# Kernel optimization log

Measured on AMD Instinct MI355X. Metric: run time of the kernel, lower is better.

## Reference

```python
import jax, jax.numpy as jnp
import numpy as np

THRESHOLD = 0.35      # overlap_thresh
NEGPOS_RATIO = 7
VAR0, VAR1 = 0.1, 0.2  # self.variance


def make_priors():
    # Standard RetinaFace 640x640 anchor grid -> 16800 priors (cx, cy, w, h)
    img = 640
    steps = [8, 16, 32]
    min_sizes = [[16, 32], [64, 128], [256, 512]]
    out = []
    for step, ms in zip(steps, min_sizes):
        f = img // step
        ii, jj = np.meshgrid(np.arange(f), np.arange(f), indexing="ij")
        cx = ((jj + 0.5) * step / img).ravel().astype(np.float32)
        cy = ((ii + 0.5) * step / img).ravel().astype(np.float32)
        for m in ms:
            s = np.full_like(cx, m / img)
            out.append(np.stack([cx, cy, s, s], axis=-1))
    return jnp.asarray(np.concatenate(out, axis=0), dtype=jnp.float32)


def jaccard(a, b):
    # a: [O,4] point-form gt boxes, b: [P,4] point-form priors -> IoU [O,P]
    lt = jnp.maximum(a[:, None, :2], b[None, :, :2])
    rb = jnp.minimum(a[:, None, 2:], b[None, :, 2:])
    wh = jnp.clip(rb - lt, 0.0)
    inter = wh[..., 0] * wh[..., 1]
    area_a = ((a[:, 2] - a[:, 0]) * (a[:, 3] - a[:, 1]))[:, None]
    area_b = ((b[:, 2] - b[:, 0]) * (b[:, 3] - b[:, 1]))[None, :]
    return inter / (area_a + area_b - inter)


def setup_inputs() -> dict:
    key = jax.random.key(0)
    ks = jax.random.split(key, 7)
    B, P, O = 64, 16800, 64
    loc_data = jax.random.normal(ks[0], (B, P, 4), jnp.float32)
    conf_data = jax.random.normal(ks[1], (B, P, 2), jnp.float32)
    landm_data = jax.random.normal(ks[2], (B, P, 10), jnp.float32)
    priors = make_priors()
    # targets: [B, O, 15] = [xmin ymin xmax ymax | 10 landmark coords | label]
    c = jax.random.uniform(ks[3], (B, O, 2), minval=0.15, maxval=0.85)
    wh = jax.random.uniform(ks[4], (B, O, 2), minval=0.05, maxval=0.3)
    boxes = jnp.concatenate([jnp.clip(c - wh / 2, 1e-3, 0.999),
                             jnp.clip(c + wh / 2, 1e-3, 0.999)], axis=-1)
    landms = jax.random.uniform(ks[5], (B, O, 10))
    lab = jnp.where(jax.random.uniform(ks[6], (B, O, 1)) < 0.8, 1.0, -1.0)
    targets = jnp.concatenate([boxes, landms, lab], axis=-1).astype(jnp.float32)
    return {"loc_data": loc_data, "conf_data": conf_data,
            "landm_data": landm_data, "priors": priors, "targets": targets}


def _smooth_l1(x):
    ax = jnp.abs(x)
    return jnp.where(ax < 1.0, 0.5 * ax * ax, ax - 0.5)


def reference(loc_data, conf_data, landm_data, priors, targets):
    B, P, C = conf_data.shape
    O = targets.shape[1]
    priors_pf = jnp.concatenate([priors[:, :2] - priors[:, 2:] * 0.5,
                                 priors[:, :2] + priors[:, 2:] * 0.5], axis=1)

    def match_one(t):
        truths = t[:, :4]
        landms = t[:, 4:14]
        labels = t[:, 14].astype(jnp.int32)
        ov = jaccard(truths, priors_pf)               # [O,P]
        bp_ov = ov.max(axis=1)                         # best prior per truth
        bp_idx = jnp.argmax(ov, axis=1)
        valid = bp_ov >= 0.2                           # RetinaFace gt filter
        bt_ov = ov.max(axis=0)                         # best truth per prior
        bt_idx = jnp.argmax(ov, axis=0)
        # index_fill_(best_prior_idx, 2) for valid gts, ensure best prior kept
        bt_ov = bt_ov.at[bp_idx].set(jnp.where(valid, 2.0, bt_ov[bp_idx]))
        bt_idx = bt_idx.at[bp_idx].set(jnp.arange(O))
        matched = truths[bt_idx]                       # [P,4] point form
        conf = labels[bt_idx]
        conf = jnp.where(bt_ov < THRESHOLD, 0, conf)
        # encode loc target
        g_cxcy = ((matched[:, :2] + matched[:, 2:]) * 0.5 - priors[:, :2]) / (VAR0 * priors[:, 2:])
        g_wh = jnp.log((matched[:, 2:] - matched[:, :2]) / priors[:, 2:]) / VAR1
        loc = jnp.concatenate([g_cxcy, g_wh], axis=1)
        # encode landmark target (5 points)
        ml = landms[bt_idx].reshape(P, 5, 2)
        lm = ((ml - priors[:, None, :2]) / (VAR0 * priors[:, None, 2:])).reshape(P, 10)
        any_valid = jnp.any(valid)                     # early-return branch of match()
        return (jnp.where(any_valid, loc, 0.0),
                jnp.where(any_valid, conf, 0),
                jnp.where(any_valid, lm, 0.0))

    loc_t, conf_t, landm_t = jax.vmap(match_one)(targets)
    loc_t = jax.lax.stop_gradient(loc_t)       # targets built from .data in torch
    landm_t = jax.lax.stop_gradient(landm_t)

    # landmark loss over conf_t > 0
    pos1 = conf_t > 0
    N1 = jnp.maximum(pos1.sum().astype(jnp.float32), 1.0)
    loss_landm = jnp.sum(jnp.where(pos1[..., None], _smooth_l1(landm_data - landm_t), 0.0))

    # localization loss over conf_t != 0 (labels -1 and 1 both positive)
    pos = conf_t != 0
    conf_t1 = jnp.where(pos, 1, conf_t)        # conf_t[pos] = 1 -> values in {0,1}
    loss_l = jnp.sum(jnp.where(pos[..., None], _smooth_l1(loc_data - loc_t), 0.0))

    # hard negative mining
    lse = jax.nn.logsumexp(conf_data, axis=2)                       # [B,P]
    picked = jnp.take_along_axis(conf_data, conf_t1[..., None], axis=2)[..., 0]
    ce_all = lse - picked                                            # per-anchor CE
    rank_score = jnp.where(pos, 0.0, ce_all)
    loss_idx = jnp.argsort(-rank_score, axis=1)
    idx_rank = jnp.argsort(loss_idx, axis=1)
    num_pos = pos.sum(axis=1, keepdims=True)
    num_neg = jnp.minimum(NEGPOS_RATIO * num_pos, P - 1)
    neg = idx_rank < num_neg
    union = pos | neg
    loss_c = jnp.sum(jnp.where(union, ce_all, 0.0))

    N = jnp.maximum(num_pos.sum().astype(jnp.float32), 1.0)
    return loss_l / N, loss_c / N, loss_landm / N1
```

## Files before the change

### kernel.cpp

```cpp
#include <hip/hip_runtime.h>
#include <math.h>

#define B 64
#define P 16800
#define O 64
#define THRESH 0.35f
#define VALID_T 0.2f
#define HB 2048
#define HSHIFT 21
#define AREA_M 0.34f
#define CCAP 4096
#define MULT 2
#define CHB (MULT * 256)
#define NB2 ((P + CHB - 1) / CHB)
#define KD1B (B * NB2)
#define KB2B (B * O / 4)

__device__ __forceinline__ float smooth_l1(float x) {
    float ax = fabsf(x);
    return ax < 1.f ? 0.5f * ax * ax : ax - 0.5f;
}
__device__ __forceinline__ float lse2(float c0, float c1) {
    float m = fmaxf(c0, c1);
    return m + __logf(__expf(c0 - m) + __expf(c1 - m));
}
__device__ __forceinline__ void iou_upd(float4 t, float area_a,
                                        float px1, float py1, float px2, float py2,
                                        float area_b,
                                        float& bnum, float& bden, int& bio, int o) {
    float w = fmaxf(fminf(t.z, px2) - fmaxf(t.x, px1), 0.f);
    float h = fmaxf(fminf(t.w, py2) - fmaxf(t.y, py1), 0.f);
    float inter = w * h;
    float den = area_a + area_b - inter;
    if (inter * bden > bnum * den) { bnum = inter; bden = den; bio = o; }
}
__device__ __forceinline__ float wave_sum(float v) {
#pragma unroll
    for (int s = 32; s > 0; s >>= 1) v += __shfl_down(v, s, 64);
    return v;
}
__device__ __forceinline__ int wave_sum_i(int v) {
#pragma unroll
    for (int s = 32; s > 0; s >>= 1) v += __shfl_down(v, s, 64);
    return v;
}
__device__ __forceinline__ float wave_min(float v) {
#pragma unroll
    for (int s = 32; s > 0; s >>= 1) v = fminf(v, __shfl_xor(v, s, 64));
    return v;
}
__device__ __forceinline__ float wave_max(float v) {
#pragma unroll
    for (int s = 32; s > 0; s >>= 1) v = fmaxf(v, __shfl_xor(v, s, 64));
    return v;
}
__device__ __forceinline__ int wave_sufscan(int v, int lane) {
#pragma unroll
    for (int s = 1; s < 64; s <<= 1) {
        int o = __shfl_down(v, s, 64);
        if (lane + s < 64) v += o;
    }
    return v;
}

__global__ void __launch_bounds__(256) kMain(
        const float* __restrict__ loc_data,
        const float* __restrict__ landm_data, const float* __restrict__ priors,
        const float* __restrict__ targets,
        unsigned char* __restrict__ pflag,
        int* __restrict__ num_pos,
        float* __restrict__ gsum, int* __restrict__ np1_tot,
        unsigned long long* __restrict__ bp_final) {
    if (blockIdx.x >= KD1B) {
        int pair = (blockIdx.x - KD1B) * 4 + (threadIdx.x >> 6);
        int lane = threadIdx.x & 63;
        int o = pair & (O - 1);
        int b = pair >> 6;
        const float* tt = &targets[(b * O + o) * 15];
        float tx1 = tt[0], ty1 = tt[1], tx2 = tt[2], ty2 = tt[3];
        float area_a = (tx2 - tx1) * (ty2 - ty1);
        float4 tb = make_float4(tx1, ty1, tx2, ty2);
        float bn = 0.f, bd = 1.f;
        unsigned bp = 0u;
        const int fs[6]   = {80, 80, 40, 40, 20, 20};
        const int ms[6]   = {16, 32, 64, 128, 256, 512};
        const int base[6] = {0, 6400, 12800, 14400, 16000, 16400};
#pragma unroll
        for (int c = 0; c < 6; ++c) {
            int f = fs[c];
            float inv = (float)f;
            float h = (float)ms[c] * (0.5f / 640.f);
            int j0 = (int)floorf((tx1 - h) * inv - 0.5f) - 1; if (j0 < 0) j0 = 0;
            int j1 = (int)ceilf((tx2 + h) * inv - 0.5f) + 1;  if (j1 > f - 1) j1 = f - 1;
            int i0 = (int)floorf((ty1 - h) * inv - 0.5f) - 1; if (i0 < 0) i0 = 0;
            int i1 = (int)ceilf((ty2 + h) * inv - 0.5f) + 1;  if (i1 > f - 1) i1 = f - 1;
            if (j1 < j0 || i1 < i0) continue;
            int nj = j1 - j0 + 1;
            int n = (i1 - i0 + 1) * nj;
            float rcp_nj = 1.0f / (float)nj;
            for (int idx = lane; idx < n; idx += 64) {
                int ii = (int)((float)idx * rcp_nj);
                int jj = idx - ii * nj;
                if (jj < 0) { ii--; jj += nj; } else if (jj >= nj) { ii++; jj -= nj; }
                int p = base[c] + (i0 + ii) * f + (j0 + jj);
                float4 q = ((const float4*)priors)[p];
                float px1 = q.x - q.z * 0.5f, py1 = q.y - q.w * 0.5f;
                float px2 = q.x + q.z * 0.5f, py2 = q.y + q.w * 0.5f;
                float areab = (px2 - px1) * (py2 - py1);
                float w = fmaxf(fminf(tb.z, px2) - fmaxf(tb.x, px1), 0.f);
                float hh = fmaxf(fminf(tb.w, py2) - fmaxf(tb.y, py1), 0.f);
                float inter = w * hh;
                float den = area_a + areab - inter;
                float l = bn * den, r = inter * bd;
                if (r > l) { bn = inter; bd = den; bp = (unsigned)p; }
            }
        }
#pragma unroll
        for (int s = 32; s > 0; s >>= 1) {
            float no = __shfl_xor(bn, s, 64), dd = __shfl_xor(bd, s, 64);
            unsigned po = __shfl_xor(bp, s, 64);
            float l = bn * dd, r = no * bd;
            bool take = (r > l) || (r == l && po < bp);
            if (take) { bn = no; bd = dd; bp = po; }
        }
        if (lane == 0) {
            float iou = bn / bd;
            bp_final[b * O + o] = ((unsigned long long)__float_as_uint(iou) << 32)
                                | (unsigned)(0xFFFFFFFFu - bp);
        }
        return;
    }
    int blk = blockIdx.x % NB2;
    int b = blockIdx.x / NB2;
    int p0 = blk * CHB;
    __shared__ float traw[O * 15];
    __shared__ float4 t4[O];
    __shared__ float ta[O], lab[O];
    __shared__ float4 wbb[4];
    __shared__ float2 wab[4];
    __shared__ int alist[O];
    __shared__ int s_cnt;
    __shared__ float wredf[2][4];
    __shared__ int wredi[2][4];
    int tid = threadIdx.x;
    if (tid < O * 15 / 4)
        ((float4*)traw)[tid] = ((const float4*)(targets + (size_t)b * O * 15))[tid];
    float px1[MULT], py1[MULT], px2[MULT], py2[MULT], areab[MULT];
    float4 pr4[MULT];
    float bnum[MULT], bden[MULT]; int bi[MULT]; bool act[MULT];
    float bx1 = 1e30f, by1 = 1e30f, bx2 = -1e30f, by2 = -1e30f;
    float amn = 1e30f, amx = -1e30f;
#pragma unroll
    for (int mi = 0; mi < MULT; ++mi) {
        int p = p0 + mi * 256 + tid;
        act[mi] = (p < P);
        int pc = act[mi] ? p : (P - 1);
        float4 q = ((const float4*)priors)[pc];
        pr4[mi] = q;
        px1[mi] = q.x - q.z * 0.5f; py1[mi] = q.y - q.w * 0.5f;
        px2[mi] = q.x + q.z * 0.5f; py2[mi] = q.y + q.w * 0.5f;
        areab[mi] = (px2[mi] - px1[mi]) * (py2[mi] - py1[mi]);
        bx1 = fminf(bx1, px1[mi]); by1 = fminf(by1, py1[mi]);
        bx2 = fmaxf(bx2, px2[mi]); by2 = fmaxf(by2, py2[mi]);
        amn = fminf(amn, areab[mi]); amx = fmaxf(amx, areab[mi]);
        bnum[mi] = 0.f; bden[mi] = 1.f; bi[mi] = 0;
    }
    bx1 = wave_min(bx1); by1 = wave_min(by1);
    bx2 = wave_max(bx2); by2 = wave_max(by2);
    amn = wave_min(amn); amx = wave_max(amx);
    int wid = tid >> 6, lid = tid & 63;
    if (lid == 0) { wbb[wid] = make_float4(bx1, by1, bx2, by2); wab[wid] = make_float2(amn, amx); }
    __syncthreads();
    if (tid < 64) {
        const float* tr = &traw[tid * 15];
        float a0 = tr[0], a1 = tr[1], a2 = tr[2], a3 = tr[3];
        float4 t = make_float4(a0, a1, a2, a3);
        t4[tid] = t;
        float Aa = (a2 - a0) * (a3 - a1);
        ta[tid] = Aa;
        lab[tid] = tr[14];
        float ux1 = fminf(fminf(wbb[0].x, wbb[1].x), fminf(wbb[2].x, wbb[3].x));
        float uy1 = fminf(fminf(wbb[0].y, wbb[1].y), fminf(wbb[2].y, wbb[3].y));
        float ux2 = fmaxf(fmaxf(wbb[0].z, wbb[1].z), fmaxf(wbb[2].z, wbb[3].z));
        float uy2 = fmaxf(fmaxf(wbb[0].w, wbb[1].w), fmaxf(wbb[2].w, wbb[3].w));
        float bmn = fminf(fminf(wab[0].x, wab[1].x), fminf(wab[2].x, wab[3].x));
        float bmx = fmaxf(fmaxf(wab[0].y, wab[1].y), fmaxf(wab[2].y, wab[3].y));
        bool pass = (fminf(t.z, ux2) - fmaxf(t.x, ux1) > 0.f) &&
                    (fminf(t.w, uy2) - fmaxf(t.y, uy1) > 0.f) &&
                    (Aa >= AREA_M * bmn) && (bmx >= AREA_M * Aa);
        unsigned long long mask = __ballot(pass);
        if (tid == 0) s_cnt = __popcll(mask);
        if (pass) {
            int pos = __popcll(mask & ((1ull << tid) - 1ull));
            alist[pos] = tid;
        }
    }
    __syncthreads();
    int cnt = s_cnt;
    for (int li = 0; li < cnt; ++li) {
        int o = alist[li];
        float4 t = t4[o];
        float w0 = fminf(t.z, bx2) - fmaxf(t.x, bx1);
        float h0 = fminf(t.w, by2) - fmaxf(t.y, by1);
        if (w0 <= 0.f || h0 <= 0.f) continue;
        float Aa = ta[o];
#pragma unroll
        for (int mi = 0; mi < MULT; ++mi) {
            float Ap = areab[mi];
            if (Aa >= AREA_M * Ap && Ap >= AREA_M * Aa)
                iou_upd(t, Aa, px1[mi], py1[mi], px2[mi], py2[mi], Ap,
                        bnum[mi], bden[mi], bi[mi], o);
        }
    }
    float ll = 0.f, llm = 0.f;
    int cp = 0, cp1 = 0;
#pragma unroll
    for (int mi = 0; mi < MULT; ++mi) {
        if (!act[mi]) continue;
        int p = p0 + mi * 256 + tid;
        float best = bnum[mi] / bden[mi];
        int conf = (best >= THRESH) ? (int)lab[bi[mi]] : 0;
        bool pos = conf != 0;
        pflag[(size_t)b * P + p] = pos ? 1 : 0;
        if (pos) {
            cp++;
            int ti = bi[mi];
            float cx = pr4[mi].x, cy = pr4[mi].y, sw = pr4[mi].z, sh = pr4[mi].w;
            float4 t = t4[ti];
            float gx = ((t.x + t.z) * 0.5f - cx) / (0.1f * sw);
            float gy = ((t.y + t.w) * 0.5f - cy) / (0.1f * sh);
            float gw = logf((t.z - t.x) / sw) / 0.2f;
            float gh = logf((t.w - t.y) / sh) / 0.2f;
            const float* ld = &loc_data[(size_t)(b * P + p) * 4];
            ll += smooth_l1(ld[0] - gx) + smooth_l1(ld[1] - gy) +
                  smooth_l1(ld[2] - gw) + smooth_l1(ld[3] - gh);
            if (conf > 0) {
                cp1++;
                const float* lmd = &landm_data[(size_t)(b * P + p) * 10];
                const float* lmt = &traw[ti * 15 + 4];
                for (int k5 = 0; k5 < 5; ++k5) {
                    float lx = (lmt[k5 * 2 + 0] - cx) / (0.1f * sw);
                    float ly = (lmt[k5 * 2 + 1] - cy) / (0.1f * sh);
                    llm += smooth_l1(lmd[k5 * 2 + 0] - lx) + smooth_l1(lmd[k5 * 2 + 1] - ly);
                }
            }
        }
    }
    float s_ll = wave_sum(ll), s_llm = wave_sum(llm);
    int s_cp = wave_sum_i(cp), s_cp1 = wave_sum_i(cp1);
    if (lid == 0) {
        wredf[0][wid] = s_ll; wredf[1][wid] = s_llm;
        wredi[0][wid] = s_cp; wredi[1][wid] = s_cp1;
    }
    __syncthreads();
    if (tid == 0) {
        float ll_t = wredf[0][0] + wredf[0][1] + wredf[0][2] + wredf[0][3];
        float llm_t = wredf[1][0] + wredf[1][1] + wredf[1][2] + wredf[1][3];
        int cp_t = wredi[0][0] + wredi[0][1] + wredi[0][2] + wredi[0][3];
        int cp1_t = wredi[1][0] + wredi[1][1] + wredi[1][2] + wredi[1][3];
        if (ll_t != 0.f)  atomicAdd(&gsum[0], ll_t);
        if (llm_t != 0.f) atomicAdd(&gsum[1], llm_t);
        if (cp_t)  atomicAdd(&num_pos[b], cp_t);
        if (cp1_t) atomicAdd(np1_tot, cp1_t);
    }
}

__global__ void __launch_bounds__(1024) kTail(
        const float* __restrict__ priors, const float* __restrict__ targets,
        const float* __restrict__ loc_data, const float* __restrict__ conf_data,
        const float* __restrict__ landm_data,
        const unsigned long long* __restrict__ bp_final,
        const unsigned char* __restrict__ pflag,
        const int* __restrict__ num_pos,
        float* __restrict__ gsum, int* __restrict__ np1_tot, int* __restrict__ np_tot,
        float* __restrict__ lossc_tot, int* __restrict__ done,
        float* __restrict__ out) {
    __shared__ __align__(16) unsigned lrow[P];
    __shared__ float4 t4[O];
    __shared__ float ta[O], lab[O];
    __shared__ int sp[O];
    __shared__ int lh[HB];
    __shared__ int chunkSum[256];
    __shared__ int suf[257];
    __shared__ int waveTot[4];
    __shared__ int hist2[256];
    __shared__ unsigned lcand[CCAP];
    __shared__ int s_np, s_bin0, s_kk0, s_bin, s_kk, s_cnt;
    __shared__ float wredf[16];
    __shared__ int wredi[16];
    __shared__ float s_cepw[16];
    __shared__ float s_sumgt;

    int b = blockIdx.x;
    int tid = threadIdx.x;
    for (int i = tid; i < HB; i += 1024) lh[i] = 0;
    if (tid == 0) s_cnt = 0;
    int p = 0, v = 0;
    if (tid < O) {
        const float* tt = &targets[(b * O + tid) * 15];
        float4 tj = make_float4(tt[0], tt[1], tt[2], tt[3]);
        t4[tid] = tj;
        ta[tid] = (tj.z - tj.x) * (tj.w - tj.y);
        lab[tid] = tt[14];
        unsigned long long kpk = bp_final[b * O + tid];
        p = (int)(0xFFFFFFFFu - (unsigned)(kpk & 0xFFFFFFFFu));
        float iou = __uint_as_float((unsigned)(kpk >> 32));
        v = (iou >= VALID_T) ? 1 : 0;
        sp[tid] = p;
    }
    __syncthreads();
    const float4* c4 = (const float4*)(conf_data + (size_t)b * P * 2);
    const uchar4* f4v = (const uchar4*)(pflag + (size_t)b * P);
    float cep = 0.f;
    for (int i = tid; i < P / 4; i += 1024) {
        float4 a = c4[2 * i];
        float4 c = c4[2 * i + 1];
        uchar4 fl = f4v[i];
        float l0 = lse2(a.x, a.y), l1 = lse2(a.z, a.w);
        float l2 = lse2(c.x, c.y), l3 = lse2(c.z, c.w);
        bool q0 = fl.x != 0, q1 = fl.y != 0, q2 = fl.z != 0, q3 = fl.w != 0;
        float ce0 = l0 - (q0 ? a.y : a.x);
        float ce1 = l1 - (q1 ? a.w : a.z);
        float ce2 = l2 - (q2 ? c.y : c.x);
        float ce3 = l3 - (q3 ? c.w : c.z);
        if (q0) cep += ce0;
        if (q1) cep += ce1;
        if (q2) cep += ce2;
        if (q3) cep += ce3;
        unsigned u0 = __float_as_uint(q0 ? 0.f : ce0);
        unsigned u1 = __float_as_uint(q1 ? 0.f : ce1);
        unsigned u2 = __float_as_uint(q2 ? 0.f : ce2);
        unsigned u3 = __float_as_uint(q3 ? 0.f : ce3);
        ((uint4*)lrow)[i] = make_uint4(u0, u1, u2, u3);
        atomicAdd(&lh[u0 >> HSHIFT], 1);
        atomicAdd(&lh[u1 >> HSHIFT], 1);
        atomicAdd(&lh[u2 >> HSHIFT], 1);
        atomicAdd(&lh[u3 >> HSHIFT], 1);
    }
    {
        float sc = wave_sum(cep);
        if ((tid & 63) == 0) s_cepw[tid >> 6] = sc;
    }
    __syncthreads();
    int dnp = 0, dn1 = 0;
    float dll = 0.f, dllm = 0.f, dce = 0.f;
    if (tid < O) {
        int j = tid;
        bool winner = true;
        for (int jj = j + 1; jj < O; ++jj)
            if (sp[jj] == p) { winner = false; break; }
        if (winner) {
            float4 q = ((const float4*)priors)[p];
            float px1 = q.x - q.z * 0.5f, py1 = q.y - q.w * 0.5f;
            float px2 = q.x + q.z * 0.5f, py2 = q.y + q.w * 0.5f;
            float areab = (px2 - px1) * (py2 - py1);
            float bnum = 0.f, bden = 1.f; int bi = 0;
            for (int o = 0; o < O; ++o) {
                float Aa = ta[o];
                if (Aa >= AREA_M * areab && areab >= AREA_M * Aa)
                    iou_upd(t4[o], Aa, px1, py1, px2, py2, areab, bnum, bden, bi, o);
            }
            float best = bnum / bden;
            float ov_new = v ? 2.0f : best;
            int conf_old = (best >= THRESH) ? (int)lab[bi] : 0;
            int conf_new = (ov_new >= THRESH) ? (int)lab[j] : 0;
            float2 c01 = ((const float2*)conf_data)[b * P + p];
            float c0 = c01.x, c1 = c01.y;
            float lse = lse2(c0, c1);
            bool po = conf_old != 0, pn = conf_new != 0;
            float ceo = lse - (po ? c1 : c0), cen = lse - (pn ? c1 : c0);
            float rvo = po ? 0.f : ceo, rvn = pn ? 0.f : cen;
            if (__float_as_uint(rvo) != __float_as_uint(rvn)) {
                lrow[p] = __float_as_uint(rvn);
                int bo = __float_as_uint(rvo) >> HSHIFT, bn = __float_as_uint(rvn) >> HSHIFT;
                if (bo != bn) { atomicAdd(&lh[bn], 1); atomicAdd(&lh[bo], -1); }
            }
            const float* ld = &loc_data[(size_t)(b * P + p) * 4];
            auto enc_ll = [&](int ti) -> float {
                float4 t = t4[ti];
                float gx = ((t.x + t.z) * 0.5f - q.x) / (0.1f * q.z);
                float gy = ((t.y + t.w) * 0.5f - q.y) / (0.1f * q.w);
                float gw = logf((t.z - t.x) / q.z) / 0.2f;
                float gh = logf((t.w - t.y) / q.w) / 0.2f;
                return smooth_l1(ld[0] - gx) + smooth_l1(ld[1] - gy) +
                       smooth_l1(ld[2] - gw) + smooth_l1(ld[3] - gh);
            };
            if (po) dll -= enc_ll(bi);
            if (pn) dll += enc_ll(j);
            dce = (pn ? cen : 0.f) - (po ? ceo : 0.f);
            dnp = (int)pn - (int)po;
            const float* lmd = &landm_data[(size_t)(b * P + p) * 10];
            auto enc_lm = [&](int ti) -> float {
                const float* lmt = &targets[(b * O + ti) * 15 + 4];
                float sum = 0.f;
                for (int k5 = 0; k5 < 5; ++k5) {
                    float lx = (lmt[k5 * 2 + 0] - q.x) / (0.1f * q.z);
                    float ly = (lmt[k5 * 2 + 1] - q.y) / (0.1f * q.w);
                    sum += smooth_l1(lmd[k5 * 2 + 0] - lx) + smooth_l1(lmd[k5 * 2 + 1] - ly);
                }
                return sum;
            };
            if (conf_old > 0) dllm -= enc_lm(bi);
            if (conf_new > 0) dllm += enc_lm(j);
            dn1 = (int)(conf_new > 0) - (int)(conf_old > 0);
        }
    }
    float pce_reg = 0.f;
    if (tid < 64) {
        float r_ll = wave_sum(dll), r_lm = wave_sum(dllm), r_ce = wave_sum(dce);
        int r_np = wave_sum_i(dnp), r_n1 = wave_sum_i(dn1);
        if (tid == 0) {
            if (r_ll != 0.f) atomicAdd(&gsum[0], r_ll);
            if (r_lm != 0.f) atomicAdd(&gsum[1], r_lm);
            float cep_tot = 0.f;
            for (int i = 0; i < 16; ++i) cep_tot += s_cepw[i];
            pce_reg = cep_tot + r_ce;
            int np = num_pos[b] + r_np;
            s_np = np;
            atomicAdd(np_tot, np);
            if (r_n1) atomicAdd(np1_tot, r_n1);
        }
    }
    __syncthreads();
    int k = s_np * 7;
    if (k > P - 1) k = P - 1;
    if (tid < 256) {
        int cs = 0;
#pragma unroll
        for (int i = 0; i < HB / 256; ++i) cs += lh[tid * (HB / 256) + i];
        chunkSum[tid] = cs;
    }
    if (tid == 0) { s_bin0 = (k <= 0) ? -1 : 0; s_kk0 = (k <= 0) ? 0 : k; }
    __syncthreads();
    {
        int lane = tid & 63;
        int vv = (tid < 256) ? chunkSum[tid] : 0;
        vv = wave_sufscan(vv, lane);
        if (tid < 256 && lane == 0) waveTot[tid >> 6] = vv;
        __syncthreads();
        if (tid < 256) {
            int after = 0;
            for (int g = (tid >> 6) + 1; g < 4; ++g) after += waveTot[g];
            suf[tid] = vv + after;
            if (tid == 0) suf[256] = 0;
        }
        __syncthreads();
        if (k > 0 && tid < 256) {
            if (suf[tid] >= k && suf[tid + 1] < k) {
                int cum = suf[tid + 1];
                for (int i = HB / 256 - 1; i >= 0; --i) {
                    int hv = lh[tid * (HB / 256) + i];
                    if (cum + hv >= k) { s_bin0 = tid * (HB / 256) + i; s_kk0 = k - cum; break; }
                    cum += hv;
                }
            }
        }
    }
    __syncthreads();
    int bin = s_bin0;
    int kk0 = s_kk0;
    float topk_b = 0.f;
    if (bin >= 0) {
        if (tid < 256) hist2[tid] = 0;
        __syncthreads();
        unsigned lo_bound = ((unsigned)(bin + 1)) << HSHIFT;
        float sumgt = 0.f;
        for (int i = tid; i < P / 4; i += 1024) {
            uint4 u4 = ((const uint4*)lrow)[i];
#define TAIL_H(u) { if ((u) >= lo_bound) sumgt += __uint_as_float(u); \
                    else if (((u) >> HSHIFT) == (unsigned)bin) { \
                        int idx = atomicAdd(&s_cnt, 1); \
                        if (idx < CCAP) lcand[idx] = (u); \
                        atomicAdd(&hist2[((u) >> 13) & 255], 1); } }
            TAIL_H(u4.x) TAIL_H(u4.y) TAIL_H(u4.z) TAIL_H(u4.w)
#undef TAIL_H
        }
        float sg = wave_sum(sumgt);
        if ((tid & 63) == 0) wredf[tid >> 6] = sg;
        __syncthreads();
        if (tid == 0) {
            float t = 0.f;
            for (int i = 0; i < 16; ++i) t += wredf[i];
            s_sumgt = t;
        }
        {
            int lane = tid & 63, nb = 256;
            int vv = (tid < nb) ? hist2[tid] : 0;
            vv = wave_sufscan(vv, lane);
            if (tid < nb && lane == 0) waveTot[tid >> 6] = vv;
            __syncthreads();
            if (tid < nb) {
                int after = 0;
                for (int g = (tid >> 6) + 1; g < 4; ++g) after += waveTot[g];
                suf[tid] = vv + after;
                if (tid == 0) suf[nb] = 0;
            }
            __syncthreads();
            if (tid < nb) {
                if (suf[tid] >= kk0 && suf[tid + 1] < kk0) { s_bin = tid; s_kk = kk0 - suf[tid + 1]; }
            }
            __syncthreads();
        }
        unsigned pref = (((unsigned)bin) << HSHIFT) | (((unsigned)s_bin) << 13);
        unsigned resolved = (0xFFFFFFFFu << HSHIFT) | (255u << 13);
        int kk = s_kk;
        int m = s_cnt;
        bool useG = (m > CCAP);
        for (int pass = 0; pass < 2; ++pass) {
            int sh = pass == 0 ? 5 : 0;
            int nb = pass == 0 ? 256 : 32;
            if (tid < nb) hist2[tid] = 0;
            __syncthreads();
            if (!useG) {
                for (int i = tid; i < m; i += 1024) {
                    unsigned u = lcand[i];
                    if ((u & resolved) == pref) atomicAdd(&hist2[(u >> sh) & (nb - 1)], 1);
                }
            } else {
                for (int pp = tid; pp < P; pp += 1024) {
                    unsigned u = lrow[pp];
                    if ((u & resolved) == pref) atomicAdd(&hist2[(u >> sh) & (nb - 1)], 1);
                }
            }
            __syncthreads();
            {
                int lane = tid & 63;
                int vv = (tid < nb) ? hist2[tid] : 0;
                vv = wave_sufscan(vv, lane);
                if (tid < nb && lane == 0) waveTot[tid >> 6] = vv;
                __syncthreads();
                int ng = (nb + 63) >> 6;
                if (tid < nb) {
                    int after = 0;
                    for (int g = (tid >> 6) + 1; g < ng; ++g) after += waveTot[g];
                    suf[tid] = vv + after;
                    if (tid == 0) suf[nb] = 0;
                }
                __syncthreads();
                if (tid < nb) {
                    if (suf[tid] >= kk && suf[tid + 1] < kk) { s_bin = tid; s_kk = kk - suf[tid + 1]; }
                }
                __syncthreads();
            }
            pref |= ((unsigned)s_bin) << sh;
            resolved |= (unsigned)(nb - 1) << sh;
            kk = s_kk;
            __syncthreads();
        }
        float tv = __uint_as_float(pref);
        float sumS = 0.f; int cntS = 0;
        for (int pp = tid; pp < P; pp += 1024) {
            unsigned u = lrow[pp];
            if ((u >> HSHIFT) == (unsigned)bin) {
                float val = __uint_as_float(u);
                if (val > tv) { sumS += val; cntS++; }
            }
        }
        float s2 = wave_sum(sumS); int c2 = wave_sum_i(cntS);
        if ((tid & 63) == 0) { wredf[tid >> 6] = s2; wredi[tid >> 6] = c2; }
        __syncthreads();
        if (tid == 0) {
            float st = 0.f; int ct = 0;
            for (int i = 0; i < 16; ++i) { st += wredf[i]; ct += wredi[i]; }
            topk_b = s_sumgt + st + (float)(kk0 - ct) * tv;
        }
    }
    if (tid == 0) {
        atomicAdd(lossc_tot, pce_reg + topk_b);
        __threadfence();
        int old = atomicAdd(done, 1);
        if (old == B - 1) {
            float g0 = atomicAdd(&gsum[0], 0.f);
            float g1 = atomicAdd(&gsum[1], 0.f);
            float lc = atomicAdd(lossc_tot, 0.f);
            int np = atomicAdd(np_tot, 0);
            int n1 = atomicAdd(np1_tot, 0);
            float N = fmaxf((float)np, 1.f);
            float N1 = fmaxf((float)n1, 1.f);
            out[0] = g0 / N;
            out[1] = lc / N;
            out[2] = g1 / N1;
        }
    }
}

extern "C" void kernel_launch(void* const* d_in, const int* in_sizes, int n_in,
                              void* d_out, int out_size, void* d_ws, size_t ws_size,
                              hipStream_t stream) {
    const float* loc_data   = (const float*)d_in[0];
    const float* conf_data  = (const float*)d_in[1];
    const float* landm_data = (const float*)d_in[2];
    const float* priors     = (const float*)d_in[3];
    const float* targets    = (const float*)d_in[4];
    float* out = (float*)d_out;

    char* ws = (char*)d_ws;
    size_t off = 0;
    auto alloc = [&](size_t bytes) -> void* {
        void* pp = ws + off;
        off += (bytes + 255) & ~(size_t)255;
        return pp;
    };
    unsigned char* pflag = (unsigned char*)alloc((size_t)B * P);
    unsigned long long* bp_final = (unsigned long long*)alloc((size_t)B * O * 8);
    size_t acc_bytes = (size_t)(B * 4 + 64);
    char* acc = (char*)alloc(acc_bytes);
    int*   num_pos      = (int*)acc;
    float* gsum         = (float*)(acc + B * 4);
    int*   np1_tot      = (int*)(acc + B * 4 + 8);
    int*   np_tot       = (int*)(acc + B * 4 + 12);
    float* lossc_tot    = (float*)(acc + B * 4 + 16);
    int*   done         = (int*)(acc + B * 4 + 20);

    hipMemsetAsync(acc, 0, acc_bytes, stream);
    kMain<<<dim3(KD1B + KB2B), dim3(256), 0, stream>>>(loc_data, landm_data,
                                                       priors, targets, pflag,
                                                       num_pos, gsum, np1_tot,
                                                       bp_final);
    kTail<<<dim3(B), dim3(1024), 0, stream>>>(priors, targets, loc_data, conf_data,
                                              landm_data, bp_final, pflag,
                                              num_pos, gsum, np1_tot, np_tot,
                                              lossc_tot, done, out);
}
```

Before: 165.4 us.

## Process two images per block, per-wave ballot culling, privatized histograms, single-wave select

The matching kernel now handles two batch rows per block and reuses the prior geometry and its per-wave bounding boxes across both rows. Candidate GT culling moves from a block-level shared list to a per-wave ballot mask over each MULT slice, which drops several barriers. The top-k kernel splits its histogram into four copies to cut atomic contention, then merges them. It also replaces the multi-barrier suffix-scan bin selection with a single-wavefront routine. Trade-offs are half as many matching blocks, so less parallelism, plus extra shared memory for the histogram copies.

```diff
diff --git a/kernel.cpp b/kernel.cpp
--- a/kernel.cpp
+++ b/kernel.cpp
@@ -11,9 +11,10 @@
 #define AREA_M 0.34f
 #define CCAP 4096
 #define MULT 2
+#define RPB 2
 #define CHB (MULT * 256)
 #define NB2 ((P + CHB - 1) / CHB)
-#define KD1B (B * NB2)
+#define KD1B ((B / RPB) * NB2)
 #define KB2B (B * O / 4)
 
 __device__ __forceinline__ float smooth_l1(float x) {
@@ -61,6 +62,27 @@
         if (lane + s < 64) v += o;
     }
     return v;
+}
+__device__ __forceinline__ void wave0_select(const int* h, int nb, int k,
+                                             int* s_bin, int* s_kk, int tid) {
+    if (tid >= 64) return;
+    int lane = tid;
+    int bpl = (nb + 63) >> 6;
+    int b0 = lane * bpl;
+    int s = 0;
+    for (int i = 0; i < bpl; ++i) { int bb = b0 + i; if (bb < nb) s += h[bb]; }
+    int suf = wave_sufscan(s, lane);
+    int sufn = __shfl_down(suf, 1, 64);
+    if (lane == 63) sufn = 0;
+    if (suf >= k && sufn < k) {
+        int cum = sufn;
+        for (int i = bpl - 1; i >= 0; --i) {
+            int bb = b0 + i; if (bb >= nb) continue;
+            int hv = h[bb];
+            if (cum + hv >= k) { *s_bin = bb; *s_kk = k - cum; break; }
+            cum += hv;
+        }
+    }
 }
 
 __global__ void __launch_bounds__(256) kMain(
@@ -131,25 +153,19 @@
         return;
     }
     int blk = blockIdx.x % NB2;
-    int b = blockIdx.x / NB2;
+    int rp = blockIdx.x / NB2;
     int p0 = blk * CHB;
     __shared__ float traw[O * 15];
     __shared__ float4 t4[O];
     __shared__ float ta[O], lab[O];
-    __shared__ float4 wbb[4];
-    __shared__ float2 wab[4];
-    __shared__ int alist[O];
-    __shared__ int s_cnt;
     __shared__ float wredf[2][4];
     __shared__ int wredi[2][4];
     int tid = threadIdx.x;
-    if (tid < O * 15 / 4)
-        ((float4*)traw)[tid] = ((const float4*)(targets + (size_t)b * O * 15))[tid];
+    int wid = tid >> 6, lid = tid & 63;
     float px1[MULT], py1[MULT], px2[MULT], py2[MULT], areab[MULT];
     float4 pr4[MULT];
-    float bnum[MULT], bden[MULT]; int bi[MULT]; bool act[MULT];
-    float bx1 = 1e30f, by1 = 1e30f, bx2 = -1e30f, by2 = -1e30f;
-    float amn = 1e30f, amx = -1e30f;
+    bool act[MULT];
+    float cbx1[MULT], cby1[MULT], cbx2[MULT], cby2[MULT], camn[MULT], camx[MULT];
 #pragma unroll
     for (int mi = 0; mi < MULT; ++mi) {
         int p = p0 + mi * 256 + tid;
@@ -160,108 +176,101 @@
         px1[mi] = q.x - q.z * 0.5f; py1[mi] = q.y - q.w * 0.5f;
         px2[mi] = q.x + q.z * 0.5f; py2[mi] = q.y + q.w * 0.5f;
         areab[mi] = (px2[mi] - px1[mi]) * (py2[mi] - py1[mi]);
-        bx1 = fminf(bx1, px1[mi]); by1 = fminf(by1, py1[mi]);
-        bx2 = fmaxf(bx2, px2[mi]); by2 = fmaxf(by2, py2[mi]);
-        amn = fminf(amn, areab[mi]); amx = fmaxf(amx, areab[mi]);
-        bnum[mi] = 0.f; bden[mi] = 1.f; bi[mi] = 0;
-    }
-    bx1 = wave_min(bx1); by1 = wave_min(by1);
-    bx2 = wave_max(bx2); by2 = wave_max(by2);
-    amn = wave_min(amn); amx = wave_max(amx);
-    int wid = tid >> 6, lid = tid & 63;
-    if (lid == 0) { wbb[wid] = make_float4(bx1, by1, bx2, by2); wab[wid] = make_float2(amn, amx); }
-    __syncthreads();
-    if (tid < 64) {
-        const float* tr = &traw[tid * 15];
-        float a0 = tr[0], a1 = tr[1], a2 = tr[2], a3 = tr[3];
-        float4 t = make_float4(a0, a1, a2, a3);
-        t4[tid] = t;
-        float Aa = (a2 - a0) * (a3 - a1);
-        ta[tid] = Aa;
-        lab[tid] = tr[14];
-        float ux1 = fminf(fminf(wbb[0].x, wbb[1].x), fminf(wbb[2].x, wbb[3].x));
-        float uy1 = fminf(fminf(wbb[0].y, wbb[1].y), fminf(wbb[2].y, wbb[3].y));
-        float ux2 = fmaxf(fmaxf(wbb[0].z, wbb[1].z), fmaxf(wbb[2].z, wbb[3].z));
-        float uy2 = fmaxf(fmaxf(wbb[0].w, wbb[1].w), fmaxf(wbb[2].w, wbb[3].w));
-        float bmn = fminf(fminf(wab[0].x, wab[1].x), fminf(wab[2].x, wab[3].x));
-        float bmx = fmaxf(fmaxf(wab[0].y, wab[1].y), fmaxf(wab[2].y, wab[3].y));
-        bool pass = (fminf(t.z, ux2) - fmaxf(t.x, ux1) > 0.f) &&
-                    (fminf(t.w, uy2) - fmaxf(t.y, uy1) > 0.f) &&
-                    (Aa >= AREA_M * bmn) && (bmx >= AREA_M * Aa);
-        unsigned long long mask = __ballot(pass);
-        if (tid == 0) s_cnt = __popcll(mask);
-        if (pass) {
-            int pos = __popcll(mask & ((1ull << tid) - 1ull));
-            alist[pos] = tid;
-        }
-    }
-    __syncthreads();
-    int cnt = s_cnt;
-    for (int li = 0; li < cnt; ++li) {
-        int o = alist[li];
-        float4 t = t4[o];
-        float w0 = fminf(t.z, bx2) - fmaxf(t.x, bx1);
-        float h0 = fminf(t.w, by2) - fmaxf(t.y, by1);
-        if (w0 <= 0.f || h0 <= 0.f) continue;
-        float Aa = ta[o];
+        cbx1[mi] = wave_min(px1[mi]); cby1[mi] = wave_min(py1[mi]);
+        cbx2[mi] = wave_max(px2[mi]); cby2[mi] = wave_max(py2[mi]);
+        camn[mi] = wave_min(areab[mi]); camx[mi] = wave_max(areab[mi]);
+    }
+    for (int r = 0; r < RPB; ++r) {
+        int b = rp * RPB + r;
+        __syncthreads();
+        if (tid < O * 15 / 4)
+            ((float4*)traw)[tid] = ((const float4*)(targets + (size_t)b * O * 15))[tid];
+        __syncthreads();
+        if (tid < 64) {
+            const float* tr = &traw[tid * 15];
+            float a0 = tr[0], a1 = tr[1], a2 = tr[2], a3 = tr[3];
+            t4[tid] = make_float4(a0, a1, a2, a3);
+            ta[tid] = (a2 - a0) * (a3 - a1);
+            lab[tid] = tr[14];
+        }
+        __syncthreads();
+        float4 tl = t4[lid];
+        float Aal = ta[lid];
+        unsigned long long mk[MULT];
 #pragma unroll
         for (int mi = 0; mi < MULT; ++mi) {
+            bool pass = (fminf(tl.z, cbx2[mi]) - fmaxf(tl.x, cbx1[mi]) > 0.f) &&
+                        (fminf(tl.w, cby2[mi]) - fmaxf(tl.y, cby1[mi]) > 0.f) &&
+                        (Aal >= AREA_M * camn[mi]) && (camx[mi] >= AREA_M * Aal);
+            mk[mi] = __ballot(pass);
+        }
+        float bnum[MULT], bden[MULT]; int bi[MULT];
+#pragma unroll
+        for (int mi = 0; mi < MULT; ++mi) {
+            bnum[mi] = 0.f; bden[mi] = 1.f; bi[mi] = 0;
+            unsigned long long mm = mk[mi];
             float Ap = areab[mi];
-            if (Aa >= AREA_M * Ap && Ap >= AREA_M * Aa)
-                iou_upd(t, Aa, px1[mi], py1[mi], px2[mi], py2[mi], Ap,
-                        bnum[mi], bden[mi], bi[mi], o);
-        }
-    }
-    float ll = 0.f, llm = 0.f;
-    int cp = 0, cp1 = 0;
-#pragma unroll
-    for (int mi = 0; mi < MULT; ++mi) {
-        if (!act[mi]) continue;
-        int p = p0 + mi * 256 + tid;
-        float best = bnum[mi] / bden[mi];
-        int conf = (best >= THRESH) ? (int)lab[bi[mi]] : 0;
-        bool pos = conf != 0;
-        pflag[(size_t)b * P + p] = pos ? 1 : 0;
-        if (pos) {
-            cp++;
-            int ti = bi[mi];
-            float cx = pr4[mi].x, cy = pr4[mi].y, sw = pr4[mi].z, sh = pr4[mi].w;
-            float4 t = t4[ti];
-            float gx = ((t.x + t.z) * 0.5f - cx) / (0.1f * sw);
-            float gy = ((t.y + t.w) * 0.5f - cy) / (0.1f * sh);
-            float gw = logf((t.z - t.x) / sw) / 0.2f;
-            float gh = logf((t.w - t.y) / sh) / 0.2f;
-            const float* ld = &loc_data[(size_t)(b * P + p) * 4];
-            ll += smooth_l1(ld[0] - gx) + smooth_l1(ld[1] - gy) +
-                  smooth_l1(ld[2] - gw) + smooth_l1(ld[3] - gh);
-            if (conf > 0) {
-                cp1++;
-                const float* lmd = &landm_data[(size_t)(b * P + p) * 10];
-                const float* lmt = &traw[ti * 15 + 4];
-                for (int k5 = 0; k5 < 5; ++k5) {
-                    float lx = (lmt[k5 * 2 + 0] - cx) / (0.1f * sw);
-                    float ly = (lmt[k5 * 2 + 1] - cy) / (0.1f * sh);
-                    llm += smooth_l1(lmd[k5 * 2 + 0] - lx) + smooth_l1(lmd[k5 * 2 + 1] - ly);
+            while (mm) {
+                int o = __ffsll(mm) - 1;
+                mm &= mm - 1;
+                float4 t = t4[o];
+                float Aa = ta[o];
+                if (Aa >= AREA_M * Ap && Ap >= AREA_M * Aa)
+                    iou_upd(t, Aa, px1[mi], py1[mi], px2[mi], py2[mi], Ap,
+                            bnum[mi], bden[mi], bi[mi], o);
+            }
+        }
+        float ll = 0.f, llm = 0.f;
+        int cp = 0, cp1 = 0;
+#pragma unroll
+        for (int mi = 0; mi < MULT; ++mi) {
+            if (!act[mi]) continue;
+            int p = p0 + mi * 256 + tid;
+            float best = bnum[mi] / bden[mi];
+            int conf = (best >= THRESH) ? (int)lab[bi[mi]] : 0;
+            bool pos = conf != 0;
+            pflag[(size_t)b * P + p] = pos ? 1 : 0;
+            if (pos) {
+                cp++;
+                int ti = bi[mi];
+                float cx = pr4[mi].x, cy = pr4[mi].y, sw = pr4[mi].z, sh = pr4[mi].w;
+                float4 t = t4[ti];
+                float gx = ((t.x + t.z) * 0.5f - cx) / (0.1f * sw);
+                float gy = ((t.y + t.w) * 0.5f - cy) / (0.1f * sh);
+                float gw = logf((t.z - t.x) / sw) / 0.2f;
+                float gh = logf((t.w - t.y) / sh) / 0.2f;
+                const float* ld = &loc_data[(size_t)(b * P + p) * 4];
+                ll += smooth_l1(ld[0] - gx) + smooth_l1(ld[1] - gy) +
+                      smooth_l1(ld[2] - gw) + smooth_l1(ld[3] - gh);
+                if (conf > 0) {
+                    cp1++;
+                    const float* lmd = &landm_data[(size_t)(b * P + p) * 10];
+                    const float* lmt = &traw[ti * 15 + 4];
+                    for (int k5 = 0; k5 < 5; ++k5) {
+                        float lx = (lmt[k5 * 2 + 0] - cx) / (0.1f * sw);
+                        float ly = (lmt[k5 * 2 + 1] - cy) / (0.1f * sh);
+                        llm += smooth_l1(lmd[k5 * 2 + 0] - lx) + smooth_l1(lmd[k5 * 2 + 1] - ly);
+                    }
                 }
             }
         }
-    }
-    float s_ll = wave_sum(ll), s_llm = wave_sum(llm);
-    int s_cp = wave_sum_i(cp), s_cp1 = wave_sum_i(cp1);
-    if (lid == 0) {
-        wredf[0][wid] = s_ll; wredf[1][wid] = s_llm;
-        wredi[0][wid] = s_cp; wredi[1][wid] = s_cp1;
-    }
-    __syncthreads();
-    if (tid == 0) {
-        float ll_t = wredf[0][0] + wredf[0][1] + wredf[0][2] + wredf[0][3];
-        float llm_t = wredf[1][0] + wredf[1][1] + wredf[1][2] + wredf[1][3];
-        int cp_t = wredi[0][0] + wredi[0][1] + wredi[0][2] + wredi[0][3];
-        int cp1_t = wredi[1][0] + wredi[1][1] + wredi[1][2] + wredi[1][3];
-        if (ll_t != 0.f)  atomicAdd(&gsum[0], ll_t);
-        if (llm_t != 0.f) atomicAdd(&gsum[1], llm_t);
-        if (cp_t)  atomicAdd(&num_pos[b], cp_t);
-        if (cp1_t) atomicAdd(np1_tot, cp1_t);
+        float s_ll = wave_sum(ll), s_llm = wave_sum(llm);
+        int s_cp = wave_sum_i(cp), s_cp1 = wave_sum_i(cp1);
+        if (lid == 0) {
+            wredf[0][wid] = s_ll; wredf[1][wid] = s_llm;
+            wredi[0][wid] = s_cp; wredi[1][wid] = s_cp1;
+        }
+        __syncthreads();
+        if (tid == 0) {
+            float ll_t = wredf[0][0] + wredf[0][1] + wredf[0][2] + wredf[0][3];
+            float llm_t = wredf[1][0] + wredf[1][1] + wredf[1][2] + wredf[1][3];
+            int cp_t = wredi[0][0] + wredi[0][1] + wredi[0][2] + wredi[0][3];
+            int cp1_t = wredi[1][0] + wredi[1][1] + wredi[1][2] + wredi[1][3];
+            if (ll_t != 0.f)  atomicAdd(&gsum[0], ll_t);
+            if (llm_t != 0.f) atomicAdd(&gsum[1], llm_t);
+            if (cp_t)  atomicAdd(&num_pos[b], cp_t);
+            if (cp1_t) atomicAdd(np1_tot, cp1_t);
+        }
     }
 }
 
@@ -276,13 +285,10 @@
         float* __restrict__ lossc_tot, int* __restrict__ done,
         float* __restrict__ out) {
     __shared__ __align__(16) unsigned lrow[P];
+    __shared__ int lh4[4][HB];
     __shared__ float4 t4[O];
     __shared__ float ta[O], lab[O];
     __shared__ int sp[O];
-    __shared__ int lh[HB];
-    __shared__ int chunkSum[256];
-    __shared__ int suf[257];
-    __shared__ int waveTot[4];
     __shared__ int hist2[256];
     __shared__ unsigned lcand[CCAP];
     __shared__ int s_np, s_bin0, s_kk0, s_bin, s_kk, s_cnt;
@@ -290,10 +296,11 @@
     __shared__ int wredi[16];
     __shared__ float s_cepw[16];
     __shared__ float s_sumgt;
+    int* lh = lh4[0];
 
     int b = blockIdx.x;
     int tid = threadIdx.x;
-    for (int i = tid; i < HB; i += 1024) lh[i] = 0;
+    for (int i = tid; i < 4 * HB; i += 1024) lh4[0][i] = 0;
     if (tid == 0) s_cnt = 0;
     int p = 0, v = 0;
     if (tid < O) {
@@ -311,6 +318,7 @@
     __syncthreads();
     const float4* c4 = (const float4*)(conf_data + (size_t)b * P * 2);
     const uchar4* f4v = (const uchar4*)(pflag + (size_t)b * P);
+    int* lhm = lh4[tid >> 8];
     float cep = 0.f;
     for (int i = tid; i < P / 4; i += 1024) {
         float4 a = c4[2 * i];
@@ -332,15 +340,18 @@
         unsigned u2 = __float_as_uint(q2 ? 0.f : ce2);
         unsigned u3 = __float_as_uint(q3 ? 0.f : ce3);
         ((uint4*)lrow)[i] = make_uint4(u0, u1, u2, u3);
-        atomicAdd(&lh[u0 >> HSHIFT], 1);
-        atomicAdd(&lh[u1 >> HSHIFT], 1);
-        atomicAdd(&lh[u2 >> HSHIFT], 1);
-        atomicAdd(&lh[u3 >> HSHIFT], 1);
+        atomicAdd(&lhm[u0 >> HSHIFT], 1);
+        atomicAdd(&lhm[u1 >> HSHIFT], 1);
+        atomicAdd(&lhm[u2 >> HSHIFT], 1);
+        atomicAdd(&lhm[u3 >> HSHIFT], 1);
     }
     {
         float sc = wave_sum(cep);
         if ((tid & 63) == 0) s_cepw[tid >> 6] = sc;
     }
+    __syncthreads();
+    for (int i = tid; i < HB; i += 1024)
+        lh[i] = lh4[0][i] + lh4[1][i] + lh4[2][i] + lh4[3][i];
     __syncthreads();
     int dnp = 0, dn1 = 0;
     float dll = 0.f, dllm = 0.f, dce = 0.f;
@@ -424,38 +435,8 @@
     __syncthreads();
     int k = s_np * 7;
     if (k > P - 1) k = P - 1;
-    if (tid < 256) {
-        int cs = 0;
-#pragma unroll
-        for (int i = 0; i < HB / 256; ++i) cs += lh[tid * (HB / 256) + i];
-        chunkSum[tid] = cs;
-    }
     if (tid == 0) { s_bin0 = (k <= 0) ? -1 : 0; s_kk0 = (k <= 0) ? 0 : k; }
-    __syncthreads();
-    {
-        int lane = tid & 63;
-        int vv = (tid < 256) ? chunkSum[tid] : 0;
-        vv = wave_sufscan(vv, lane);
-        if (tid < 256 && lane == 0) waveTot[tid >> 6] = vv;
-        __syncthreads();
-        if (tid < 256) {
-            int after = 0;
-            for (int g = (tid >> 6) + 1; g < 4; ++g) after += waveTot[g];
-            suf[tid] = vv + after;
-            if (tid == 0) suf[256] = 0;
-        }
-        __syncthreads();
-        if (k > 0 && tid < 256) {
-            if (suf[tid] >= k && suf[tid + 1] < k) {
-                int cum = suf[tid + 1];
-                for (int i = HB / 256 - 1; i >= 0; --i) {
-                    int hv = lh[tid * (HB / 256) + i];
-                    if (cum + hv >= k) { s_bin0 = tid * (HB / 256) + i; s_kk0 = k - cum; break; }
-                    cum += hv;
-                }
-            }
-        }
-    }
+    if (k > 0) wave0_select(lh, HB, k, &s_bin0, &s_kk0, tid);
     __syncthreads();
     int bin = s_bin0;
     int kk0 = s_kk0;
@@ -483,24 +464,8 @@
             for (int i = 0; i < 16; ++i) t += wredf[i];
             s_sumgt = t;
         }
-        {
-            int lane = tid & 63, nb = 256;
-            int vv = (tid < nb) ? hist2[tid] : 0;
-            vv = wave_sufscan(vv, lane);
-            if (tid < nb && lane == 0) waveTot[tid >> 6] = vv;
-            __syncthreads();
-            if (tid < nb) {
-                int after = 0;
-                for (int g = (tid >> 6) + 1; g < 4; ++g) after += waveTot[g];
-                suf[tid] = vv + after;
-                if (tid == 0) suf[nb] = 0;
-            }
-            __syncthreads();
-            if (tid < nb) {
-                if (suf[tid] >= kk0 && suf[tid + 1] < kk0) { s_bin = tid; s_kk = kk0 - suf[tid + 1]; }
-            }
-            __syncthreads();
-        }
+        wave0_select(hist2, 256, kk0, &s_bin, &s_kk, tid);
+        __syncthreads();
         unsigned pref = (((unsigned)bin) << HSHIFT) | (((unsigned)s_bin) << 13);
         unsigned resolved = (0xFFFFFFFFu << HSHIFT) | (255u << 13);
         int kk = s_kk;
@@ -523,29 +488,11 @@
                 }
             }
             __syncthreads();
-            {
-                int lane = tid & 63;
-                int vv = (tid < nb) ? hist2[tid] : 0;
-                vv = wave_sufscan(vv, lane);
-                if (tid < nb && lane == 0) waveTot[tid >> 6] = vv;
-                __syncthreads();
-                int ng = (nb + 63) >> 6;
-                if (tid < nb) {
-                    int after = 0;
-                    for (int g = (tid >> 6) + 1; g < ng; ++g) after += waveTot[g];
-                    suf[tid] = vv + after;
-                    if (tid == 0) suf[nb] = 0;
-                }
-                __syncthreads();
-                if (tid < nb) {
-                    if (suf[tid] >= kk && suf[tid + 1] < kk) { s_bin = tid; s_kk = kk - suf[tid + 1]; }
-                }
-                __syncthreads();
-            }
+            wave0_select(hist2, nb, kk, &s_bin, &s_kk, tid);
+            __syncthreads();
             pref |= ((unsigned)s_bin) << sh;
             resolved |= (unsigned)(nb - 1) << sh;
             kk = s_kk;
-            __syncthreads();
         }
         float tv = __uint_as_float(pref);
         float sumS = 0.f; int cntS = 0;
```

Result: no change. 165.6 us (+0.1%).
